# Kernel tuning notes

Hardware: AMD Instinct MI355X
Metric: run time of the kernel (lower is better)

Reference implementation:

```python
import jax, jax.numpy as jnp
import numpy as np

B, T, DIN, DOUT = 2, 2048, 1024, 1024
G, H = 4, 16
HPG = H // G          # heads per group = 4
DH = DOUT // H        # head dim = 64
THETA = 10000.0


def _rope_tables(t, dh):
    inv_freq = 1.0 / (THETA ** (np.arange(0, dh, 2, dtype=np.float32) / dh))
    pos = np.arange(t, dtype=np.float32)
    freqs = np.outer(pos, inv_freq)              # [T, DH/2]
    emb = np.concatenate([freqs, freqs], axis=-1)  # [T, DH]
    return jnp.asarray(np.cos(emb)), jnp.asarray(np.sin(emb))


def _rotate_half(x):
    x1, x2 = jnp.split(x, 2, axis=-1)
    return jnp.concatenate([-x2, x1], axis=-1)


def setup_inputs() -> dict:
    key = jax.random.key(0)
    ks = jax.random.split(key, 5)
    s = 0.02
    x = jax.random.normal(ks[0], (B, T, DIN), jnp.float32)
    Wq = jax.random.normal(ks[1], (DIN, DOUT), jnp.float32) * s
    Wk = jax.random.normal(ks[2], (DIN, G * DH), jnp.float32) * s
    Wv = jax.random.normal(ks[3], (DIN, G * DH), jnp.float32) * s
    Wo = jax.random.normal(ks[4], (DOUT, DOUT), jnp.float32) * s
    cos, sin = _rope_tables(T, DH)
    return {"x": x, "Wq": Wq, "Wk": Wk, "Wv": Wv, "Wo": Wo, "cos": cos, "sin": sin}


def reference(x, Wq, Wk, Wv, Wo, cos, sin):
    b, t, _ = x.shape
    # projections
    q = (x @ Wq).reshape(b, t, G, HPG, DH).transpose(0, 2, 1, 3, 4)  # [B,G,T,Hpg,DH]
    k = (x @ Wk).reshape(b, t, G, DH).transpose(0, 2, 1, 3)           # [B,G,T,DH]
    v = (x @ Wv).reshape(b, t, G, DH).transpose(0, 2, 1, 3)           # [B,G,T,DH]
    # RoPE (cos/sin [T,DH]; for q broadcast over Hpg via extra axis)
    q = q * cos[:, None, :] + _rotate_half(q) * sin[:, None, :]
    k = k * cos + _rotate_half(k) * sin
    q = q.transpose(0, 1, 3, 2, 4)  # [B,G,Hpg,T,DH]
    # scores [B,G,Hpg,T,T]
    scores = jnp.einsum('bghtd,bgsd->bghts', q, k)
    causal = jnp.triu(jnp.ones((t, t), bool), k=1)
    scores = jnp.where(causal, -jnp.inf, scores)
    # NOTE: original code divides by sqrt(token_len), not sqrt(head_dim)
    attn = jax.nn.softmax(scores / jnp.float32(t) ** 0.5, axis=-1)
    out = jnp.einsum('bghts,bgsd->bghtd', attn, v)     # [B,G,Hpg,T,DH]
    out = out.transpose(0, 3, 1, 2, 4).reshape(b, t, DOUT)
    return out @ Wo
```

## Files before the change

kernel.cpp:

```cpp
#include <hip/hip_runtime.h>
#include <hip/hip_bf16.h>

typedef __attribute__((ext_vector_type(8))) short short8;
typedef __attribute__((ext_vector_type(4))) float f32x4;
typedef __attribute__((ext_vector_type(16))) float f32x16;

#define T_    2048
#define QKVN  1536
#define DOUT_ 1024

__device__ __forceinline__ unsigned short bf16r(float f) {
    union { float f; unsigned u; } v; v.f = f;
    unsigned r = v.u + 0x7fffu + ((v.u >> 16) & 1u);
    return (unsigned short)(r >> 16);
}
__device__ __forceinline__ float fbf16(short s) {
    union { unsigned u; float f; } v; v.u = ((unsigned)(unsigned short)s) << 16;
    return v.f;
}
__device__ __forceinline__ void plswap(unsigned &a, unsigned &b) {
    asm volatile("v_permlane32_swap_b32 %0, %1" : "+v"(a), "+v"(b));
}
__device__ __forceinline__ unsigned cvtpk(float lo, float hi) {
    unsigned r;
    asm("v_cvt_pk_bf16_f32 %0, %1, %2" : "=v"(r) : "v"(lo), "v"(hi));
    return r;
}
__device__ __forceinline__ void gload_lds16(const void* g, void* l) {
    __builtin_amdgcn_global_load_lds(
        (const __attribute__((address_space(1))) void*)g,
        (__attribute__((address_space(3))) void*)l, 16, 0, 0);
}

__global__ __launch_bounds__(256)
void k_prep(const float* __restrict__ x, const float* __restrict__ Wq,
            const float* __restrict__ Wk, const float* __restrict__ Wv,
            const float* __restrict__ Wo, short* __restrict__ XB,
            short* __restrict__ WT, short* __restrict__ WoT) {
    __shared__ short tile[64][72];
    int blk = blockIdx.x;
    int t = threadIdx.x;
    if (blk >= 640) {
        int i = (blk - 640) * 256 + t;
#pragma unroll
        for (int rep = 0; rep < 2; rep++, i += 262144) {
            const float* s = x + (size_t)i * 8;
            float4 f1 = *(const float4*)s;
            float4 f2 = *(const float4*)(s + 4);
            uint4 o;
            o.x = (unsigned)bf16r(f1.x) | ((unsigned)bf16r(f1.y) << 16);
            o.y = (unsigned)bf16r(f1.z) | ((unsigned)bf16r(f1.w) << 16);
            o.z = (unsigned)bf16r(f2.x) | ((unsigned)bf16r(f2.y) << 16);
            o.w = (unsigned)bf16r(f2.z) | ((unsigned)bf16r(f2.w) << 16);
            *(uint4*)(XB + (size_t)i * 8) = o;
        }
        return;
    }
    const float* src; short* dst; int N, bx, by;
    if (blk < 256)      { src = Wq; dst = WT;              N = 1024; bx = blk & 15;         by = blk >> 4; }
    else if (blk < 320) { src = Wk; dst = WT + 1024*1024;  N = 256;  bx = (blk-256) & 15;   by = (blk-256) >> 4; }
    else if (blk < 384) { src = Wv; dst = WT + 1280*1024;  N = 256;  bx = (blk-320) & 15;   by = (blk-320) >> 4; }
    else                { src = Wo; dst = WoT;             N = 1024; bx = (blk-384) & 15;   by = (blk-384) >> 4; }
    const int K = 1024;
    int tk = bx * 64, tn = by * 64;
    int r4 = t >> 6, c = t & 63;
#pragma unroll
    for (int i = 0; i < 16; i++) {
        int row = i * 4 + r4;
        tile[c][row] = (short)bf16r(src[(size_t)(tk + row) * N + tn + c]);
    }
    __syncthreads();
    int row = t >> 2, seg = t & 3;
    short8 a = *(const short8*)&tile[row][seg * 16];
    short8 b = *(const short8*)&tile[row][seg * 16 + 8];
    *(short8*)&dst[(size_t)(tn + row) * K + tk + seg * 16]     = a;
    *(short8*)&dst[(size_t)(tn + row) * K + tk + seg * 16 + 8] = b;
}

__global__ __launch_bounds__(256)
void k_vt(const short* __restrict__ qkv, short* __restrict__ vt) {
    __shared__ short tile[64][72];
    int bid = blockIdx.x;
    int b = bid & 1, g = (bid >> 1) & 3, tt = bid >> 3;
    int t0v = tt * 64;
    int tid = threadIdx.x;
    int row = tid >> 2, sp = tid & 3;
    const short* src = qkv + ((size_t)(b * T_ + t0v + row) * QKVN + 1280 + g * 64 + sp * 16);
    uint4 a = *(const uint4*)src;
    uint4 c2 = *(const uint4*)(src + 8);
    const short* ap = (const short*)&a;
    const short* cp = (const short*)&c2;
#pragma unroll
    for (int x = 0; x < 8; x++) tile[sp * 16 + x][row]     = ap[x];
#pragma unroll
    for (int x = 0; x < 8; x++) tile[sp * 16 + 8 + x][row] = cp[x];
    __syncthreads();
    int d = tid >> 2;
    short* dst = vt + ((size_t)((b * 4 + g) * 64 + d) * T_ + t0v + sp * 16);
    *(uint4*)dst       = *(const uint4*)&tile[d][sp * 16];
    *(uint4*)(dst + 8) = *(const uint4*)&tile[d][sp * 16 + 8];
}

template <int CF32, int ROPE>
__global__ __launch_bounds__(256, 4)
void k_gemm(const short* __restrict__ A, const short* __restrict__ Bt,
            void* __restrict__ Cv, int M, int N, int K,
            const float* __restrict__ cosT, const float* __restrict__ sinT) {
    __shared__ __align__(16) short As[64][64];
    __shared__ __align__(16) short Bs[128][64];
    int tid = threadIdx.x;
    int l = tid & 63, w = tid >> 6;
    int lr = l & 15, lg = l >> 4;
    int m0 = blockIdx.x * 64;
    int n0 = blockIdx.y * 128;
    int wr = (w >> 1) * 32, wc = (w & 1) * 64;
    int lrow = l >> 3;
    int lsw  = (((l & 7) ^ (lrow & 7)) << 3);
    int rx   = lr & 7;

    f32x4 z = {0.f, 0.f, 0.f, 0.f};
    f32x4 acc[2][4];
#pragma unroll
    for (int m = 0; m < 2; m++)
#pragma unroll
        for (int n = 0; n < 4; n++) acc[m][n] = z;

    for (int k0 = 0; k0 < K; k0 += 64) {
#pragma unroll
        for (int i = 0; i < 2; i++) {
            int ch = w * 2 + i;
            gload_lds16(A + (size_t)(m0 + ch * 8 + lrow) * K + k0 + lsw,
                        &As[ch * 8][0]);
        }
#pragma unroll
        for (int i = 0; i < 4; i++) {
            int ch = w * 4 + i;
            gload_lds16(Bt + (size_t)(n0 + ch * 8 + lrow) * K + k0 + lsw,
                        &Bs[ch * 8][0]);
        }
        __syncthreads();
#pragma unroll
        for (int kk = 0; kk < 2; kk++) {
            int jd = kk * 4 + lg;
            int gg = (jd ^ rx) << 3;
            short8 af[2], bf[4];
#pragma unroll
            for (int m = 0; m < 2; m++)
                af[m] = *(const short8*)&As[wr + m * 16 + lr][gg];
#pragma unroll
            for (int n = 0; n < 4; n++)
                bf[n] = *(const short8*)&Bs[wc + n * 16 + lr][gg];
#pragma unroll
            for (int m = 0; m < 2; m++)
#pragma unroll
                for (int n = 0; n < 4; n++)
                    acc[m][n] = __builtin_amdgcn_mfma_f32_16x16x32_bf16(
                        af[m], bf[n], acc[m][n], 0, 0, 0);
        }
        __syncthreads();
    }
#pragma unroll
    for (int m = 0; m < 2; m++)
#pragma unroll
        for (int r = 0; r < 4; r++) {
            int row = m0 + wr + m * 16 + lg * 4 + r;
            if (ROPE) {
                int h = (n0 + wc) >> 6;
                if (h < 20) {
                    int t = row & (T_ - 1);
#pragma unroll
                    for (int n = 0; n < 2; n++) {
                        int d = n * 16 + lr;
                        float cd = cosT[t * 64 + d];
                        float sd = sinT[t * 64 + d];
                        float a = acc[m][n][r], bb = acc[m][n + 2][r];
                        acc[m][n][r]     = a * cd - bb * sd;
                        acc[m][n + 2][r] = bb * cd + a * sd;
                    }
                }
            }
#pragma unroll
            for (int n = 0; n < 4; n++) {
                int col = n0 + wc + n * 16 + lr;
                float v = acc[m][n][r];
                if (CF32) ((float*)Cv)[(size_t)row * N + col] = v;
                else      ((short*)Cv)[(size_t)row * N + col] = (short)bf16r(v);
            }
        }
}

__global__ __launch_bounds__(256, 4)
void k_attn(const short* __restrict__ qkv, const short* __restrict__ vt,
            short* __restrict__ opart, float* __restrict__ lpart) {
    __shared__ __align__(16) short KsL[2][4096];
    __shared__ __align__(16) short VsL[2][4096];
    int id = blockIdx.x;
    int bg = id & 7;
    int vv = 159 - (id >> 3);
    int qt, c, nc;
    if (vv < 64) { qt = vv >> 1; c = vv & 1; nc = 2; }
    else { int v2 = vv - 64; qt = 32 + (v2 & 31); c = v2 >> 5; nc = 3; }
    int slot = bg * 160 + vv;
    int b = bg & 1, g = (bg >> 1) & 3;
    int q0 = qt * 32;
    int nt = (qt + 2) >> 1;
    int t0 = c * nt / nc, t1 = (c + 1) * nt / nc;

    int tid = threadIdx.x;
    int w = tid >> 6;
    int l = tid & 63;
    int lc = l & 31, hi = l >> 5;
    const float s2 = 0.03187928f;
    size_t rowbase = (size_t)b * T_ * QKVN;
    int qcol = g * 256 + w * 64;
    int kcol = 1024 + g * 64;
    const short* vbase = vt + (size_t)((b * 4 + g) * 64) * T_;

    short8 qf[4];
#pragma unroll
    for (int dkk = 0; dkk < 4; dkk++) {
        short8 raw = *(const short8*)(qkv + rowbase + (size_t)(q0 + lc) * QKVN
                                      + qcol + dkk * 16 + hi * 8);
        short8 sc;
#pragma unroll
        for (int x = 0; x < 8; x++) sc[x] = (short)bf16r(fbf16(raw[x]) * s2);
        qf[dkk] = sc;
    }

    const short one_bf = (short)0x3F80;
    short8 ones8 = {one_bf, one_bf, one_bf, one_bf, one_bf, one_bf, one_bf, one_bf};

    int C0 = (w * 2) * 64 + l, C1 = (w * 2 + 1) * 64 + l;
    int r0 = C0 >> 3, j0 = (C0 & 7) ^ (r0 & 7);
    int r1 = C1 >> 3, j1 = (C1 & 7) ^ (r1 & 7);
    const short* kA0 = qkv + rowbase + (size_t)(t0 * 64 + r0) * QKVN + kcol + j0 * 8;
    const short* kA1 = qkv + rowbase + (size_t)(t0 * 64 + r1) * QKVN + kcol + j1 * 8;
    const short* vA0 = vbase + (size_t)r0 * T_ + t0 * 64 + j0 * 8;
    const short* vA1 = vbase + (size_t)r1 * T_ + t0 * 64 + j1 * 8;
    auto STAGE = [&](int bu) {
        gload_lds16(kA0, &KsL[bu][(w * 2) * 512]);
        gload_lds16(kA1, &KsL[bu][(w * 2 + 1) * 512]);
        gload_lds16(vA0, &VsL[bu][(w * 2) * 512]);
        gload_lds16(vA1, &VsL[bu][(w * 2 + 1) * 512]);
        kA0 += 64 * QKVN; kA1 += 64 * QKVN; vA0 += 64; vA1 += 64;
    };

    f32x16 Z16 = {0.f,0.f,0.f,0.f,0.f,0.f,0.f,0.f,0.f,0.f,0.f,0.f,0.f,0.f,0.f,0.f};
    f32x16 acc[2];
    acc[0] = Z16; acc[1] = Z16;
    f32x16 lac = Z16;

    if (t0 < t1) STAGE(0);
    for (int kt = t0; kt < t1; kt++) {
        int bu = (kt - t0) & 1;
        int s0 = kt * 64;
        bool last = (kt == nt - 1);
        __syncthreads();
        if (kt + 1 < t1) STAGE(bu ^ 1);

#pragma unroll
        for (int kf = 0; kf < 2; kf++) {
            f32x16 s = Z16;
            __builtin_amdgcn_s_setprio(1);
#pragma unroll
            for (int dkk = 0; dkk < 4; dkk++) {
                int r = kf * 32 + lc;
                int jd = dkk * 2 + hi;
                short8 ka = *(const short8*)&KsL[bu][r * 64 + ((jd ^ (r & 7)) << 3)];
                s = __builtin_amdgcn_mfma_f32_32x32x16_bf16(ka, qf[dkk], s, 0, 0, 0);
            }
            __builtin_amdgcn_s_setprio(0);
            float p[16];
            if (last) {
                int qrow = q0 + lc;
                int kb = s0 + kf * 32 + hi * 4;
#pragma unroll
                for (int reg = 0; reg < 16; reg++) {
                    int key = kb + (reg & 3) + ((reg >> 2) << 3);
                    p[reg] = (key <= qrow) ? exp2f(s[reg]) : 0.f;
                }
            } else {
#pragma unroll
                for (int reg = 0; reg < 16; reg++) p[reg] = exp2f(s[reg]);
            }
            unsigned pk[4][2];
#pragma unroll
            for (int sb = 0; sb < 4; sb++) {
                pk[sb][0] = cvtpk(p[4 * sb],     p[4 * sb + 1]);
                pk[sb][1] = cvtpk(p[4 * sb + 2], p[4 * sb + 3]);
            }
            __builtin_amdgcn_s_setprio(1);
#pragma unroll
            for (int kk = 0; kk < 2; kk++) {
                unsigned a0 = pk[2 * kk][0], b0 = pk[2 * kk + 1][0];
                unsigned a1 = pk[2 * kk][1], b1 = pk[2 * kk + 1][1];
                plswap(a0, b0);
                plswap(a1, b1);
                union { unsigned u[4]; short8 s8; } pb;
                pb.u[0] = a0; pb.u[1] = a1; pb.u[2] = b0; pb.u[3] = b1;
#pragma unroll
                for (int df = 0; df < 2; df++) {
                    int r = df * 32 + lc;
                    int jk = kf * 4 + kk * 2 + hi;
                    short8 va = *(const short8*)&VsL[bu][r * 64 + ((jk ^ (r & 7)) << 3)];
                    acc[df] = __builtin_amdgcn_mfma_f32_32x32x16_bf16(va, pb.s8, acc[df], 0, 0, 0);
                }
                lac = __builtin_amdgcn_mfma_f32_32x32x16_bf16(ones8, pb.s8, lac, 0, 0, 0);
            }
            __builtin_amdgcn_s_setprio(0);
        }
    }

    float lt = lac[0];

    short* ob = opart + (size_t)slot * 8192 + lc * 256 + w * 64;
#pragma unroll
    for (int df = 0; df < 2; df++)
#pragma unroll
        for (int sb = 0; sb < 4; sb++) {
            unsigned u0 = cvtpk(acc[df][4 * sb],     acc[df][4 * sb + 1]);
            unsigned u1 = cvtpk(acc[df][4 * sb + 2], acc[df][4 * sb + 3]);
            uint2 uv = {u0, u1};
            *(uint2*)(ob + df * 32 + sb * 8 + hi * 4) = uv;
        }
    if (hi == 0) lpart[slot * 128 + lc * 4 + w] = lt;
}

__global__ __launch_bounds__(256)
void k_comb(const short* __restrict__ opart, const float* __restrict__ lpart,
            short* __restrict__ attn) {
    int id = blockIdx.x;
    int bg = id & 7, qt = id >> 3;
    int b = bg & 1, g = (bg >> 1) & 3;
    int t = threadIdx.x;
    int row = t >> 3, s = t & 7;
    int head = s >> 1, colseg = s * 32;
    int nc = (qt < 32) ? 2 : 3;
    float acc[32];
#pragma unroll
    for (int i = 0; i < 32; i++) acc[i] = 0.f;
    float lsum = 0.f;
    for (int c = 0; c < nc; c++) {
        int vv = (qt < 32) ? (2 * qt + c) : (64 + (qt - 32) + 32 * c);
        int oid = bg * 160 + vv;
        lsum += lpart[oid * 128 + row * 4 + head];
        const short* ob = opart + (size_t)oid * 8192 + row * 256 + colseg;
#pragma unroll
        for (int i = 0; i < 4; i++) {
            uint4 v = *(const uint4*)(ob + i * 8);
            const short* vs = (const short*)&v;
#pragma unroll
            for (int j = 0; j < 8; j++) acc[i * 8 + j] += fbf16(vs[j]);
        }
    }
    float inv = 1.0f / lsum;
    unsigned out[16];
#pragma unroll
    for (int i = 0; i < 16; i++)
        out[i] = cvtpk(acc[2 * i] * inv, acc[2 * i + 1] * inv);
    short* dst = attn + ((size_t)(b * T_ + qt * 32 + row)) * DOUT_ + g * 256 + colseg;
#pragma unroll
    for (int i = 0; i < 4; i++) *(uint4*)(dst + i * 8) = *(const uint4*)&out[i * 4];
}

extern "C" void kernel_launch(void* const* d_in, const int* in_sizes, int n_in,
                              void* d_out, int out_size, void* d_ws, size_t ws_size,
                              hipStream_t stream) {
    const float* x    = (const float*)d_in[0];
    const float* Wq   = (const float*)d_in[1];
    const float* Wk   = (const float*)d_in[2];
    const float* Wv   = (const float*)d_in[3];
    const float* Wo   = (const float*)d_in[4];
    const float* cosT = (const float*)d_in[5];
    const float* sinT = (const float*)d_in[6];

    char* ws = (char*)d_ws;
    short* WT    = (short*)(ws);
    short* WoT   = (short*)(ws + 3145728);
    short* QKV   = (short*)(ws + 5242880);
    short* ATT   = (short*)(ws + 17825792);
    short* VT    = (short*)(ws + 26214400);
    short* XB    = (short*)(ws + 28311552);
    short* OPART = (short*)(ws + 28311552);
    float* LPART = (float*)(ws + 49283072);

    k_prep<<<1664, 256, 0, stream>>>(x, Wq, Wk, Wv, Wo, XB, WT, WoT);
    k_gemm<0, 1><<<dim3(64, 12), 256, 0, stream>>>(XB, WT, (void*)QKV,
                                                   4096, 1536, 1024, cosT, sinT);
    k_vt<<<256, 256, 0, stream>>>(QKV, VT);
    k_attn<<<1280, 256, 0, stream>>>(QKV, VT, OPART, LPART);
    k_comb<<<512, 256, 0, stream>>>(OPART, LPART, ATT);
    k_gemm<1, 0><<<dim3(64, 8), 256, 0, stream>>>(ATT, WoT, d_out,
                                                  4096, 1024, 1024, nullptr, nullptr);
}
```

Before: 96.01 us.

## Share K/V tiles across two query tiles with 512-thread attention blocks

Each attention block now has 8 waves covering two adjacent 32-row query tiles (64 query rows) that share the same staged K/V tiles in LDS, so each K/V tile is loaded once per 64 query rows rather than once per 32. The split-K work decomposition and the combine kernel's slot indexing are reworked to match, and waves of the first query tile skip the fully masked half of the diagonal tile. This cuts global/LDS staging traffic and halves the block count, but larger blocks may reduce scheduling flexibility and tail balance.

```diff
diff --git a/kernel.cpp b/kernel.cpp
--- a/kernel.cpp
+++ b/kernel.cpp
@@ -189,30 +189,33 @@
         }
 }
 
-__global__ __launch_bounds__(256, 4)
+__global__ __launch_bounds__(512, 6)
 void k_attn(const short* __restrict__ qkv, const short* __restrict__ vt,
             short* __restrict__ opart, float* __restrict__ lpart) {
     __shared__ __align__(16) short KsL[2][4096];
     __shared__ __align__(16) short VsL[2][4096];
     int id = blockIdx.x;
     int bg = id & 7;
-    int vv = 159 - (id >> 3);
-    int qt, c, nc;
-    if (vv < 64) { qt = vv >> 1; c = vv & 1; nc = 2; }
-    else { int v2 = vv - 64; qt = 32 + (v2 & 31); c = v2 >> 5; nc = 3; }
-    int slot = bg * 160 + vv;
+    int j0 = id >> 3;
+    {
+    }
+    int j = j0, k = 31, c;
+    for (;;) { int ncK = (k + 8) >> 3; if (j < ncK) { c = j; break; } j -= ncK; k--; }
+    int ncK = (k + 8) >> 3;
+    int nt = k + 1;
+    int t0 = c * nt / ncK, t1 = (c + 1) * nt / ncK;
     int b = bg & 1, g = (bg >> 1) & 3;
-    int q0 = qt * 32;
-    int nt = (qt + 2) >> 1;
-    int t0 = c * nt / nc, t1 = (c + 1) * nt / nc;
 
     int tid = threadIdx.x;
     int w = tid >> 6;
+    int hq = w & 3, grp = w >> 2;
+    int slot = bg * 160 + j0 * 2 + grp;
+    int q0 = k * 64 + grp * 32;
     int l = tid & 63;
     int lc = l & 31, hi = l >> 5;
     const float s2 = 0.03187928f;
     size_t rowbase = (size_t)b * T_ * QKVN;
-    int qcol = g * 256 + w * 64;
+    int qcol = g * 256 + hq * 64;
     int kcol = 1024 + g * 64;
     const short* vbase = vt + (size_t)((b * 4 + g) * 64) * T_;
 
@@ -230,19 +233,14 @@
     const short one_bf = (short)0x3F80;
     short8 ones8 = {one_bf, one_bf, one_bf, one_bf, one_bf, one_bf, one_bf, one_bf};
 
-    int C0 = (w * 2) * 64 + l, C1 = (w * 2 + 1) * 64 + l;
-    int r0 = C0 >> 3, j0 = (C0 & 7) ^ (r0 & 7);
-    int r1 = C1 >> 3, j1 = (C1 & 7) ^ (r1 & 7);
-    const short* kA0 = qkv + rowbase + (size_t)(t0 * 64 + r0) * QKVN + kcol + j0 * 8;
-    const short* kA1 = qkv + rowbase + (size_t)(t0 * 64 + r1) * QKVN + kcol + j1 * 8;
-    const short* vA0 = vbase + (size_t)r0 * T_ + t0 * 64 + j0 * 8;
-    const short* vA1 = vbase + (size_t)r1 * T_ + t0 * 64 + j1 * 8;
+    int C = (w << 6) + l;
+    int r0 = C >> 3, jj0 = (C & 7) ^ (r0 & 7);
+    const short* kA = qkv + rowbase + (size_t)(t0 * 64 + r0) * QKVN + kcol + jj0 * 8;
+    const short* vA = vbase + (size_t)r0 * T_ + t0 * 64 + jj0 * 8;
     auto STAGE = [&](int bu) {
-        gload_lds16(kA0, &KsL[bu][(w * 2) * 512]);
-        gload_lds16(kA1, &KsL[bu][(w * 2 + 1) * 512]);
-        gload_lds16(vA0, &VsL[bu][(w * 2) * 512]);
-        gload_lds16(vA1, &VsL[bu][(w * 2 + 1) * 512]);
-        kA0 += 64 * QKVN; kA1 += 64 * QKVN; vA0 += 64; vA1 += 64;
+        gload_lds16(kA, &KsL[bu][w * 512]);
+        gload_lds16(vA, &VsL[bu][w * 512]);
+        kA += 64 * QKVN; vA += 64;
     };
 
     f32x16 Z16 = {0.f,0.f,0.f,0.f,0.f,0.f,0.f,0.f,0.f,0.f,0.f,0.f,0.f,0.f,0.f,0.f};
@@ -250,7 +248,7 @@
     acc[0] = Z16; acc[1] = Z16;
     f32x16 lac = Z16;
 
-    if (t0 < t1) STAGE(0);
+    STAGE(0);
     for (int kt = t0; kt < t1; kt++) {
         int bu = (kt - t0) & 1;
         int s0 = kt * 64;
@@ -260,6 +258,7 @@
 
 #pragma unroll
         for (int kf = 0; kf < 2; kf++) {
+            if (last && grp == 0 && kf == 1) break;
             f32x16 s = Z16;
             __builtin_amdgcn_s_setprio(1);
 #pragma unroll
@@ -313,7 +312,7 @@
 
     float lt = lac[0];
 
-    short* ob = opart + (size_t)slot * 8192 + lc * 256 + w * 64;
+    short* ob = opart + (size_t)slot * 8192 + lc * 256 + hq * 64;
 #pragma unroll
     for (int df = 0; df < 2; df++)
 #pragma unroll
@@ -323,7 +322,7 @@
             uint2 uv = {u0, u1};
             *(uint2*)(ob + df * 32 + sb * 8 + hi * 4) = uv;
         }
-    if (hi == 0) lpart[slot * 128 + lc * 4 + w] = lt;
+    if (hi == 0) lpart[slot * 128 + lc * 4 + hq] = lt;
 }
 
 __global__ __launch_bounds__(256)
@@ -332,17 +331,19 @@
     int id = blockIdx.x;
     int bg = id & 7, qt = id >> 3;
     int b = bg & 1, g = (bg >> 1) & 3;
+    int k = qt >> 1, grp = qt & 1;
+    int base = 0;
+    for (int kk = 31; kk > k; kk--) base += (kk + 8) >> 3;
+    int ncK = (k + 8) >> 3;
     int t = threadIdx.x;
     int row = t >> 3, s = t & 7;
     int head = s >> 1, colseg = s * 32;
-    int nc = (qt < 32) ? 2 : 3;
     float acc[32];
 #pragma unroll
     for (int i = 0; i < 32; i++) acc[i] = 0.f;
     float lsum = 0.f;
-    for (int c = 0; c < nc; c++) {
-        int vv = (qt < 32) ? (2 * qt + c) : (64 + (qt - 32) + 32 * c);
-        int oid = bg * 160 + vv;
+    for (int c = 0; c < ncK; c++) {
+        int oid = bg * 160 + (base + c) * 2 + grp;
         lsum += lpart[oid * 128 + row * 4 + head];
         const short* ob = opart + (size_t)oid * 8192 + row * 256 + colseg;
 #pragma unroll
@@ -388,7 +389,7 @@
     k_gemm<0, 1><<<dim3(64, 12), 256, 0, stream>>>(XB, WT, (void*)QKV,
                                                    4096, 1536, 1024, cosT, sinT);
     k_vt<<<256, 256, 0, stream>>>(QKV, VT);
-    k_attn<<<1280, 256, 0, stream>>>(QKV, VT, OPART, LPART);
+    k_attn<<<640, 512, 0, stream>>>(QKV, VT, OPART, LPART);
     k_comb<<<512, 256, 0, stream>>>(OPART, LPART, ATT);
     k_gemm<1, 0><<<dim3(64, 8), 256, 0, stream>>>(ATT, WoT, d_out,
                                                   4096, 1024, 1024, nullptr, nullptr);
```

New measurement: 208.5 us. 117% more time.
